# Kernel tuning notes

Measured on AMD Instinct MI355X. Metric: run time of the kernel, lower is better.

## Reference

```python
import jax, jax.numpy as jnp
import numpy as np

HID = 1024
HEADS = 16
HEAD_DIM = HID // HEADS
SCALE = HEAD_DIM ** -0.5


def setup_inputs() -> dict:
    key = jax.random.key(0)
    ks = jax.random.split(key, 11)
    B, S = 4, 2048
    std = HID ** -0.5
    inp = {
        'q': jax.random.normal(ks[0], (B, S, HID), jnp.float32),
        'k': jax.random.normal(ks[1], (B, S, HID), jnp.float32),
        'v': jax.random.normal(ks[2], (B, S, HID), jnp.float32),
        'Wq': jax.random.normal(ks[3], (HID, HID), jnp.float32) * std,
        'bq': jnp.zeros((HID,), jnp.float32),
        'Wk': jax.random.normal(ks[4], (HID, HID), jnp.float32) * std,
        'bk': jnp.zeros((HID,), jnp.float32),
        'Wv': jax.random.normal(ks[5], (HID, HID), jnp.float32) * std,
        'bv': jnp.zeros((HID,), jnp.float32),
        'Wo': jax.random.normal(ks[6], (HID, HID), jnp.float32) * std,
        'bo': jnp.zeros((HID,), jnp.float32),
    }
    return inp


def _split_heads(x, B):
    # [B, S, HID] -> [B, H, S, Dh]
    return x.reshape(B, -1, HEADS, HEAD_DIM).transpose(0, 2, 1, 3)


def reference(q, k, v, Wq, bq, Wk, bk, Wv, bv, Wo, bo):
    B = q.shape[0]
    Q = _split_heads(jnp.dot(q, Wq.T) + bq, B)
    K = _split_heads(jnp.dot(k, Wk.T) + bk, B)
    V = _split_heads(jnp.dot(v, Wv.T) + bv, B)
    # [B, H, Sq, Sk]
    energy = jnp.einsum('bhqd,bhkd->bhqk', Q, K) * SCALE
    attention = jax.nn.softmax(energy, axis=-1)
    x = jnp.einsum('bhqk,bhkd->bhqd', attention, V)  # dropout = identity (eval)
    x = x.transpose(0, 2, 1, 3).reshape(B, -1, HID)
    x = jnp.dot(x, Wo.T) + bo
    return (x, attention)
```

## Files before the change

kernel.cpp:

```cpp
#include <hip/hip_runtime.h>
#include <stdint.h>

#define HID 1024
#define HEADS 16
#define HDIM 64
#define SEQ 2048
#define BATCH 4
#define SCALE 0.125f
#define EXPC 0.18033688011112042f

typedef __bf16 bf16x8 __attribute__((ext_vector_type(8)));
typedef float f32x4 __attribute__((ext_vector_type(4)));
typedef unsigned short ushortx8 __attribute__((ext_vector_type(8)));
typedef unsigned short ushortx4 __attribute__((ext_vector_type(4)));

__device__ __forceinline__ unsigned short f2bf(float f) {
  uint32_t u = __builtin_bit_cast(uint32_t, f);
  u = (u + 0x7fffu + ((u >> 16) & 1u)) >> 16;
  return (unsigned short)u;
}
__device__ __forceinline__ float bf2f(unsigned short u) {
  uint32_t x = ((uint32_t)u) << 16;
  return __builtin_bit_cast(float, x);
}
__device__ __forceinline__ void gl16(const void* g, void* l) {
  __builtin_amdgcn_global_load_lds(
      (const __attribute__((address_space(1))) unsigned int*)g,
      (__attribute__((address_space(3))) unsigned int*)l, 16, 0, 0);
}

struct ConvArgs {
  const float* s[6];
  unsigned short* d[6];
  int n[6];
};
__global__ __launch_bounds__(256) void convk(ConvArgs a) {
  const int ten = blockIdx.y;
  const float* s = a.s[ten];
  unsigned short* d = a.d[ten];
  const int n = a.n[ten];
  const int stride = gridDim.x * blockDim.x * 8;
  for (int i = (blockIdx.x * blockDim.x + threadIdx.x) * 8; i < n; i += stride) {
    float4 v0 = *(const float4*)(s + i);
    float4 v1 = *(const float4*)(s + i + 4);
    ushortx8 o = {f2bf(v0.x), f2bf(v0.y), f2bf(v0.z), f2bf(v0.w),
                  f2bf(v1.x), f2bf(v1.y), f2bf(v1.z), f2bf(v1.w)};
    *(ushortx8*)(d + i) = o;
  }
}

template <int W_F32, int OUT_MODE>
__global__ __launch_bounds__(256) void gemm_bf(
    const unsigned short* __restrict__ A, const void* __restrict__ Wp,
    const float* __restrict__ bias, void* __restrict__ Out) {
  __shared__ unsigned short Als[128 * 64];
  __shared__ unsigned short Bls[128 * 64];
  const int t = threadIdx.x;
  const int bn = blockIdx.x, bm = blockIdx.y;
  const int w = t >> 6, lane = t & 63;
  const int wm = w >> 1, wn = w & 1;
  const int lr = lane & 15, lk = lane >> 4;
  const int row0 = bm * 128, col0 = bn * 128;

  const unsigned short* Abase =
      A + (size_t)(row0 + w * 32 + (lane >> 3)) * HID + (lane & 7) * 8;
  const unsigned short* Wb16 =
      (const unsigned short*)Wp + (size_t)(col0 + w * 32 + (lane >> 3)) * HID +
      (lane & 7) * 8;

  f32x4 acc[4][4] = {};

  for (int ks = 0; ks < 16; ++ks) {
    __syncthreads();
#pragma unroll
    for (int i = 0; i < 4; ++i)
      gl16(Abase + (size_t)i * 8 * HID + ks * 64, &Als[(w * 32 + i * 8) * 64]);
    if (!W_F32) {
#pragma unroll
      for (int i = 0; i < 4; ++i)
        gl16(Wb16 + (size_t)i * 8 * HID + ks * 64, &Bls[(w * 32 + i * 8) * 64]);
    } else {
      const float* Wf = (const float*)Wp;
#pragma unroll
      for (int i = 0; i < 8; ++i) {
        int chunk = t + i * 256;
        int r = chunk >> 4, c4 = (chunk & 15) * 4;
        float4 v4 = *(const float4*)(Wf + (size_t)(col0 + r) * HID + ks * 64 + c4);
        ushortx4 o = {f2bf(v4.x), f2bf(v4.y), f2bf(v4.z), f2bf(v4.w)};
        *(ushortx4*)&Bls[r * 64 + c4] = o;
      }
    }
    __syncthreads();
#pragma unroll
    for (int kk = 0; kk < 2; ++kk) {
      bf16x8 a[4], bb[4];
#pragma unroll
      for (int f = 0; f < 4; ++f) {
        a[f] = *(const bf16x8*)&Als[(wm * 64 + f * 16 + lr) * 64 + kk * 32 + lk * 8];
        bb[f] = *(const bf16x8*)&Bls[(wn * 64 + f * 16 + lr) * 64 + kk * 32 + lk * 8];
      }
#pragma unroll
      for (int fm = 0; fm < 4; ++fm)
#pragma unroll
        for (int fn = 0; fn < 4; ++fn)
          acc[fm][fn] = __builtin_amdgcn_mfma_f32_16x16x32_bf16(
              a[fm], bb[fn], acc[fm][fn], 0, 0, 0);
    }
  }

#pragma unroll
  for (int fn = 0; fn < 4; ++fn) {
    int col = col0 + wn * 64 + fn * 16 + lr;
    float bv = bias[col];
#pragma unroll
    for (int fm = 0; fm < 4; ++fm) {
      int row = row0 + wm * 64 + fm * 16 + lk * 4;
      if (OUT_MODE == 1) {
        int b_ = row >> 11, s = row & 2047;
        int hh = col >> 6, d = col & 63;
        ushortx4 o4 = {f2bf(acc[fm][fn][0] + bv), f2bf(acc[fm][fn][1] + bv),
                       f2bf(acc[fm][fn][2] + bv), f2bf(acc[fm][fn][3] + bv)};
        *(ushortx4*)((unsigned short*)Out +
                     ((size_t)(b_ * HEADS + hh) * HDIM + d) * SEQ + s) = o4;
      } else {
#pragma unroll
        for (int r = 0; r < 4; ++r) {
          float v = acc[fm][fn][r] + bv;
          if (OUT_MODE == 0)
            ((unsigned short*)Out)[(size_t)(row + r) * HID + col] = f2bf(v);
          else
            ((float*)Out)[(size_t)(row + r) * HID + col] = v;
        }
      }
    }
  }
}

__global__ __launch_bounds__(512) void attn_kern(
    const unsigned short* __restrict__ Qb, const unsigned short* __restrict__ Kb,
    const unsigned short* __restrict__ Vt, float* __restrict__ attn_out,
    unsigned short* __restrict__ Xc) {
  __shared__ unsigned short Qls[128][72];
  __shared__ unsigned short Kls[2][64 * 64];
  __shared__ unsigned short Vls[2][64 * 64];

  const int t = threadIdx.x;
  const int qb = blockIdx.x, h = blockIdx.y, b = blockIdx.z;
  const int w = t >> 6, lane = t & 63;
  const int lr = lane & 15, lk = lane >> 4;
  const size_t qrow0 = (size_t)b * SEQ + (size_t)qb * 128;

  const int srow = lane >> 3;
  const int scol = (lane & 7) ^ srow;
  const unsigned short* gK =
      Kb + ((size_t)b * SEQ + w * 8 + srow) * HID + h * HDIM + scol * 8;
  const unsigned short* gV =
      Vt + ((size_t)(b * HEADS + h) * HDIM + w * 8 + srow) * SEQ + scol * 8;
  unsigned short* lK = &Kls[0][w * 8 * 64];
  unsigned short* lV = &Vls[0][w * 8 * 64];

  gl16(gK, lK);

#pragma unroll
  for (int i = 0; i < 2; ++i) {
    int chunk = t + i * 512;
    int r = chunk >> 3, c8 = (chunk & 7) * 8;
    *(ushortx8*)&Qls[r][c8] =
        *(const ushortx8*)(Qb + (qrow0 + r) * HID + h * HDIM + c8);
  }
  __syncthreads();

  bf16x8 qf[2];
#pragma unroll
  for (int kk = 0; kk < 2; ++kk)
    qf[kk] = *(const bf16x8*)&Qls[w * 16 + lr][kk * 32 + lk * 8];
  auto& Pls = Qls;

  float lsum[4] = {0.f, 0.f, 0.f, 0.f};
  int buf = 0;

  for (int kt = 0; kt < 32; ++kt) {
    if (kt < 31) gl16(gK + (size_t)(kt + 1) * 64 * HID, lK + (buf ^ 1) * 4096);
    f32x4 acc[4] = {};
    __builtin_amdgcn_s_setprio(1);
#pragma unroll
    for (int kk = 0; kk < 2; ++kk)
#pragma unroll
      for (int kf = 0; kf < 4; ++kf) {
        bf16x8 bb = *(const bf16x8*)&Kls[buf][(kf * 16 + lr) * 64 +
                                             (((kk * 4 + lk) ^ (lr & 7)) << 3)];
        acc[kf] = __builtin_amdgcn_mfma_f32_16x16x32_bf16(qf[kk], bb, acc[kf], 0, 0, 0);
      }
    __builtin_amdgcn_s_setprio(0);
#pragma unroll
    for (int kf = 0; kf < 4; ++kf)
#pragma unroll
      for (int r = 0; r < 4; ++r) lsum[r] += exp2f(acc[kf][r] * EXPC);
    __syncthreads();
    buf ^= 1;
  }

  float invl[4];
#pragma unroll
  for (int r = 0; r < 4; ++r) {
#pragma unroll
    for (int off = 1; off < 16; off <<= 1) lsum[r] += __shfl_xor(lsum[r], off, 64);
    invl[r] = 1.0f / lsum[r];
  }

  f32x4 oacc[4] = {};
  float* attn_base =
      attn_out + ((size_t)(b * HEADS + h) * SEQ + (size_t)qb * 128) * SEQ;

  gl16(gK, lK);
  gl16(gV, lV);
  __syncthreads();
  for (int kt = 0; kt < 32; ++kt) {
    if (kt < 31) {
      gl16(gK + (size_t)(kt + 1) * 64 * HID, lK + (buf ^ 1) * 4096);
      gl16(gV + (size_t)(kt + 1) * 64, lV + (buf ^ 1) * 4096);
    }
    f32x4 acc[4] = {};
    __builtin_amdgcn_s_setprio(1);
#pragma unroll
    for (int kk = 0; kk < 2; ++kk)
#pragma unroll
      for (int kf = 0; kf < 4; ++kf) {
        bf16x8 bb = *(const bf16x8*)&Kls[buf][(kf * 16 + lr) * 64 +
                                             (((kk * 4 + lk) ^ (lr & 7)) << 3)];
        acc[kf] = __builtin_amdgcn_mfma_f32_16x16x32_bf16(qf[kk], bb, acc[kf], 0, 0, 0);
      }
    __builtin_amdgcn_s_setprio(0);
#pragma unroll
    for (int kf = 0; kf < 4; ++kf)
#pragma unroll
      for (int r = 0; r < 4; ++r) {
        float p = exp2f(acc[kf][r] * EXPC) * invl[r];
        Pls[w * 16 + lk * 4 + r][kf * 16 + lr] = f2bf(p);
      }
#pragma unroll
    for (int it = 0; it < 4; ++it) {
      int rl = it * 4 + lk;
      ushortx4 p4 = *(const ushortx4*)&Pls[w * 16 + rl][lr * 4];
      f32x4 o = {bf2f(p4[0]), bf2f(p4[1]), bf2f(p4[2]), bf2f(p4[3])};
      __builtin_nontemporal_store(
          o, (f32x4*)(attn_base + (size_t)(w * 16 + rl) * SEQ + kt * 64 + lr * 4));
    }
    __builtin_amdgcn_s_setprio(1);
#pragma unroll
    for (int kk = 0; kk < 2; ++kk) {
      bf16x8 ap = *(const bf16x8*)&Pls[w * 16 + lr][kk * 32 + lk * 8];
#pragma unroll
      for (int df = 0; df < 4; ++df) {
        bf16x8 bv = *(const bf16x8*)&Vls[buf][(df * 16 + lr) * 64 +
                                             (((kk * 4 + lk) ^ (lr & 7)) << 3)];
        oacc[df] = __builtin_amdgcn_mfma_f32_16x16x32_bf16(ap, bv, oacc[df], 0, 0, 0);
      }
    }
    __builtin_amdgcn_s_setprio(0);
    __syncthreads();
    buf ^= 1;
  }

#pragma unroll
  for (int df = 0; df < 4; ++df)
#pragma unroll
    for (int r = 0; r < 4; ++r) {
      int row = w * 16 + lk * 4 + r;
      int col = h * HDIM + df * 16 + lr;
      Xc[(qrow0 + row) * HID + col] = f2bf(oacc[df][r]);
    }
}

extern "C" void kernel_launch(void* const* d_in, const int* in_sizes, int n_in,
                              void* d_out, int out_size, void* d_ws, size_t ws_size,
                              hipStream_t stream) {
  const float* q = (const float*)d_in[0];
  const float* k = (const float*)d_in[1];
  const float* v = (const float*)d_in[2];
  const float* Wq = (const float*)d_in[3];
  const float* bq = (const float*)d_in[4];
  const float* Wk = (const float*)d_in[5];
  const float* bk = (const float*)d_in[6];
  const float* Wv = (const float*)d_in[7];
  const float* bv = (const float*)d_in[8];
  const float* Wo = (const float*)d_in[9];
  const float* bo = (const float*)d_in[10];

  char* ws = (char*)d_ws;
  const size_t MAT = (size_t)8192 * 1024 * sizeof(unsigned short);
  unsigned short* Qbuf = (unsigned short*)(ws);
  unsigned short* Kbuf = (unsigned short*)(ws + MAT);
  unsigned short* Vtb = (unsigned short*)(ws + 2 * MAT);
  unsigned short* Xc = (unsigned short*)(ws + 3 * MAT);

  float* xout = (float*)d_out;
  float* attn_out = xout + (size_t)BATCH * SEQ * HID;

  unsigned short* scr = (unsigned short*)attn_out;
  const int NQ = 8192 * 1024, NW = 1024 * 1024;
  unsigned short* qb16 = scr;
  unsigned short* kb16 = scr + (size_t)NQ;
  unsigned short* vb16 = scr + (size_t)2 * NQ;
  unsigned short* wq16 = scr + (size_t)3 * NQ;
  unsigned short* wk16 = wq16 + NW;
  unsigned short* wv16 = wk16 + NW;

  ConvArgs ca;
  ca.s[0] = q; ca.s[1] = k; ca.s[2] = v; ca.s[3] = Wq; ca.s[4] = Wk; ca.s[5] = Wv;
  ca.d[0] = qb16; ca.d[1] = kb16; ca.d[2] = vb16;
  ca.d[3] = wq16; ca.d[4] = wk16; ca.d[5] = wv16;
  ca.n[0] = NQ; ca.n[1] = NQ; ca.n[2] = NQ;
  ca.n[3] = NW; ca.n[4] = NW; ca.n[5] = NW;

  dim3 blk(256);
  hipLaunchKernelGGL(convk, dim3(512, 6), blk, 0, stream, ca);
  dim3 gp(8, 64);
  hipLaunchKernelGGL((gemm_bf<0, 0>), gp, blk, 0, stream, qb16, wq16, bq, Qbuf);
  hipLaunchKernelGGL((gemm_bf<0, 0>), gp, blk, 0, stream, kb16, wk16, bk, Kbuf);
  hipLaunchKernelGGL((gemm_bf<0, 1>), gp, blk, 0, stream, vb16, wv16, bv, Vtb);
  hipLaunchKernelGGL((attn_kern), dim3(16, 16, 4), dim3(512), 0, stream, Qbuf, Kbuf,
                     Vtb, attn_out, Xc);
  hipLaunchKernelGGL((gemm_bf<1, 2>), gp, blk, 0, stream, Xc, Wo, bo, xout);
}
```

Measured before the change: 460.4 us.

## Merge QKV GEMMs, remap attention blocks per XCD, pre-convert Wo to bf16

```diff
diff --git a/kernel.cpp b/kernel.cpp
--- a/kernel.cpp
+++ b/kernel.cpp
@@ -30,9 +30,9 @@
 }
 
 struct ConvArgs {
-  const float* s[6];
-  unsigned short* d[6];
-  int n[6];
+  const float* s[7];
+  unsigned short* d[7];
+  int n[7];
 };
 __global__ __launch_bounds__(256) void convk(ConvArgs a) {
   const int ten = blockIdx.y;
@@ -49,10 +49,87 @@
   }
 }
 
-template <int W_F32, int OUT_MODE>
-__global__ __launch_bounds__(256) void gemm_bf(
+struct QkvArgs {
+  const unsigned short* A[3];
+  const unsigned short* W[3];
+  const float* bias[3];
+  unsigned short* out[3];
+};
+__global__ __launch_bounds__(256) void gemm_qkv(QkvArgs ar) {
+  __shared__ unsigned short Als[128 * 64];
+  __shared__ unsigned short Bls[128 * 64];
+  const int z = blockIdx.z;
+  const unsigned short* A = ar.A[z];
+  const unsigned short* Wb = ar.W[z];
+  const float* bias = ar.bias[z];
+  unsigned short* Out = ar.out[z];
+
+  const int t = threadIdx.x;
+  const int bn = blockIdx.x, bm = blockIdx.y;
+  const int w = t >> 6, lane = t & 63;
+  const int wm = w >> 1, wn = w & 1;
+  const int lr = lane & 15, lk = lane >> 4;
+  const int row0 = bm * 128, col0 = bn * 128;
+
+  const unsigned short* Abase =
+      A + (size_t)(row0 + w * 32 + (lane >> 3)) * HID + (lane & 7) * 8;
+  const unsigned short* Wbase =
+      Wb + (size_t)(col0 + w * 32 + (lane >> 3)) * HID + (lane & 7) * 8;
+
+  f32x4 acc[4][4] = {};
+
+  for (int ks = 0; ks < 16; ++ks) {
+    __syncthreads();
+#pragma unroll
+    for (int i = 0; i < 4; ++i)
+      gl16(Abase + (size_t)i * 8 * HID + ks * 64, &Als[(w * 32 + i * 8) * 64]);
+#pragma unroll
+    for (int i = 0; i < 4; ++i)
+      gl16(Wbase + (size_t)i * 8 * HID + ks * 64, &Bls[(w * 32 + i * 8) * 64]);
+    __syncthreads();
+#pragma unroll
+    for (int kk = 0; kk < 2; ++kk) {
+      bf16x8 a[4], bb[4];
+#pragma unroll
+      for (int f = 0; f < 4; ++f) {
+        a[f] = *(const bf16x8*)&Als[(wm * 64 + f * 16 + lr) * 64 + kk * 32 + lk * 8];
+        bb[f] = *(const bf16x8*)&Bls[(wn * 64 + f * 16 + lr) * 64 + kk * 32 + lk * 8];
+      }
+#pragma unroll
+      for (int fm = 0; fm < 4; ++fm)
+#pragma unroll
+        for (int fn = 0; fn < 4; ++fn)
+          acc[fm][fn] = __builtin_amdgcn_mfma_f32_16x16x32_bf16(
+              a[fm], bb[fn], acc[fm][fn], 0, 0, 0);
+    }
+  }
+
+#pragma unroll
+  for (int fn = 0; fn < 4; ++fn) {
+    int col = col0 + wn * 64 + fn * 16 + lr;
+    float bv = bias[col];
+#pragma unroll
+    for (int fm = 0; fm < 4; ++fm) {
+      int row = row0 + wm * 64 + fm * 16 + lk * 4;
+      if (z == 2) {
+        int b_ = row >> 11, s = row & 2047;
+        int hh = col >> 6, d = col & 63;
+        ushortx4 o4 = {f2bf(acc[fm][fn][0] + bv), f2bf(acc[fm][fn][1] + bv),
+                       f2bf(acc[fm][fn][2] + bv), f2bf(acc[fm][fn][3] + bv)};
+        *(ushortx4*)(Out + ((size_t)(b_ * HEADS + hh) * HDIM + d) * SEQ + s) = o4;
+      } else {
+#pragma unroll
+        for (int r = 0; r < 4; ++r)
+          Out[(size_t)(row + r) * HID + col] = f2bf(acc[fm][fn][r] + bv);
+      }
+    }
+  }
+}
+
+template <int W_F32>
+__global__ __launch_bounds__(256) void gemm_wo(
     const unsigned short* __restrict__ A, const void* __restrict__ Wp,
-    const float* __restrict__ bias, void* __restrict__ Out) {
+    const float* __restrict__ bias, float* __restrict__ Out) {
   __shared__ unsigned short Als[128 * 64];
   __shared__ unsigned short Bls[128 * 64];
   const int t = threadIdx.x;
@@ -115,23 +192,9 @@
 #pragma unroll
     for (int fm = 0; fm < 4; ++fm) {
       int row = row0 + wm * 64 + fm * 16 + lk * 4;
-      if (OUT_MODE == 1) {
-        int b_ = row >> 11, s = row & 2047;
-        int hh = col >> 6, d = col & 63;
-        ushortx4 o4 = {f2bf(acc[fm][fn][0] + bv), f2bf(acc[fm][fn][1] + bv),
-                       f2bf(acc[fm][fn][2] + bv), f2bf(acc[fm][fn][3] + bv)};
-        *(ushortx4*)((unsigned short*)Out +
-                     ((size_t)(b_ * HEADS + hh) * HDIM + d) * SEQ + s) = o4;
-      } else {
-#pragma unroll
-        for (int r = 0; r < 4; ++r) {
-          float v = acc[fm][fn][r] + bv;
-          if (OUT_MODE == 0)
-            ((unsigned short*)Out)[(size_t)(row + r) * HID + col] = f2bf(v);
-          else
-            ((float*)Out)[(size_t)(row + r) * HID + col] = v;
-        }
-      }
+#pragma unroll
+      for (int r = 0; r < 4; ++r)
+        Out[(size_t)(row + r) * HID + col] = acc[fm][fn][r] + bv;
     }
   }
 }
@@ -145,10 +208,14 @@
   __shared__ unsigned short Vls[2][64 * 64];
 
   const int t = threadIdx.x;
-  const int qb = blockIdx.x, h = blockIdx.y, b = blockIdx.z;
+  const int bid = blockIdx.x;
+  const int wgid = (bid & 7) * 64 + (bid >> 3);
+  const int qbp = wgid & 7;
+  const int h = (wgid >> 3) & 15;
+  const int b = wgid >> 7;
+
   const int w = t >> 6, lane = t & 63;
   const int lr = lane & 15, lk = lane >> 4;
-  const size_t qrow0 = (size_t)b * SEQ + (size_t)qb * 128;
 
   const int srow = lane >> 3;
   const int scol = (lane & 7) ^ srow;
@@ -159,117 +226,123 @@
   unsigned short* lK = &Kls[0][w * 8 * 64];
   unsigned short* lV = &Vls[0][w * 8 * 64];
 
-  gl16(gK, lK);
-
-#pragma unroll
-  for (int i = 0; i < 2; ++i) {
-    int chunk = t + i * 512;
-    int r = chunk >> 3, c8 = (chunk & 7) * 8;
-    *(ushortx8*)&Qls[r][c8] =
-        *(const ushortx8*)(Qb + (qrow0 + r) * HID + h * HDIM + c8);
-  }
-  __syncthreads();
-
-  bf16x8 qf[2];
-#pragma unroll
-  for (int kk = 0; kk < 2; ++kk)
-    qf[kk] = *(const bf16x8*)&Qls[w * 16 + lr][kk * 32 + lk * 8];
-  auto& Pls = Qls;
-
-  float lsum[4] = {0.f, 0.f, 0.f, 0.f};
-  int buf = 0;
-
-  for (int kt = 0; kt < 32; ++kt) {
-    if (kt < 31) gl16(gK + (size_t)(kt + 1) * 64 * HID, lK + (buf ^ 1) * 4096);
-    f32x4 acc[4] = {};
-    __builtin_amdgcn_s_setprio(1);
+  for (int qbi = 0; qbi < 2; ++qbi) {
+    const int qb = qbp * 2 + qbi;
+    const size_t qrow0 = (size_t)b * SEQ + (size_t)qb * 128;
+
+    gl16(gK, lK);
+#pragma unroll
+    for (int i = 0; i < 2; ++i) {
+      int chunk = t + i * 512;
+      int r = chunk >> 3, c8 = (chunk & 7) * 8;
+      *(ushortx8*)&Qls[r][c8] =
+          *(const ushortx8*)(Qb + (qrow0 + r) * HID + h * HDIM + c8);
+    }
+    __syncthreads();
+
+    bf16x8 qf[2];
 #pragma unroll
     for (int kk = 0; kk < 2; ++kk)
-#pragma unroll
-      for (int kf = 0; kf < 4; ++kf) {
-        bf16x8 bb = *(const bf16x8*)&Kls[buf][(kf * 16 + lr) * 64 +
-                                             (((kk * 4 + lk) ^ (lr & 7)) << 3)];
-        acc[kf] = __builtin_amdgcn_mfma_f32_16x16x32_bf16(qf[kk], bb, acc[kf], 0, 0, 0);
-      }
-    __builtin_amdgcn_s_setprio(0);
-#pragma unroll
-    for (int kf = 0; kf < 4; ++kf)
-#pragma unroll
-      for (int r = 0; r < 4; ++r) lsum[r] += exp2f(acc[kf][r] * EXPC);
-    __syncthreads();
-    buf ^= 1;
-  }
-
-  float invl[4];
-#pragma unroll
-  for (int r = 0; r < 4; ++r) {
-#pragma unroll
-    for (int off = 1; off < 16; off <<= 1) lsum[r] += __shfl_xor(lsum[r], off, 64);
-    invl[r] = 1.0f / lsum[r];
-  }
-
-  f32x4 oacc[4] = {};
-  float* attn_base =
-      attn_out + ((size_t)(b * HEADS + h) * SEQ + (size_t)qb * 128) * SEQ;
-
-  gl16(gK, lK);
-  gl16(gV, lV);
-  __syncthreads();
-  for (int kt = 0; kt < 32; ++kt) {
-    if (kt < 31) {
-      gl16(gK + (size_t)(kt + 1) * 64 * HID, lK + (buf ^ 1) * 4096);
-      gl16(gV + (size_t)(kt + 1) * 64, lV + (buf ^ 1) * 4096);
-    }
-    f32x4 acc[4] = {};
-    __builtin_amdgcn_s_setprio(1);
-#pragma unroll
-    for (int kk = 0; kk < 2; ++kk)
-#pragma unroll
-      for (int kf = 0; kf < 4; ++kf) {
-        bf16x8 bb = *(const bf16x8*)&Kls[buf][(kf * 16 + lr) * 64 +
-                                             (((kk * 4 + lk) ^ (lr & 7)) << 3)];
-        acc[kf] = __builtin_amdgcn_mfma_f32_16x16x32_bf16(qf[kk], bb, acc[kf], 0, 0, 0);
-      }
-    __builtin_amdgcn_s_setprio(0);
-#pragma unroll
-    for (int kf = 0; kf < 4; ++kf)
+      qf[kk] = *(const bf16x8*)&Qls[w * 16 + lr][kk * 32 + lk * 8];
+    auto& Pls = Qls;
+
+    float lsum[4] = {0.f, 0.f, 0.f, 0.f};
+    int buf = 0;
+
+    for (int kt = 0; kt < 32; ++kt) {
+      if (kt < 31) gl16(gK + (size_t)(kt + 1) * 64 * HID, lK + (buf ^ 1) * 4096);
+      f32x4 acc[4] = {};
+      __builtin_amdgcn_s_setprio(1);
+#pragma unroll
+      for (int kk = 0; kk < 2; ++kk)
+#pragma unroll
+        for (int kf = 0; kf < 4; ++kf) {
+          bf16x8 bb = *(const bf16x8*)&Kls[buf][(kf * 16 + lr) * 64 +
+                                               (((kk * 4 + lk) ^ (lr & 7)) << 3)];
+          acc[kf] =
+              __builtin_amdgcn_mfma_f32_16x16x32_bf16(qf[kk], bb, acc[kf], 0, 0, 0);
+        }
+      __builtin_amdgcn_s_setprio(0);
+#pragma unroll
+      for (int kf = 0; kf < 4; ++kf)
+#pragma unroll
+        for (int r = 0; r < 4; ++r) lsum[r] += exp2f(acc[kf][r] * EXPC);
+      __syncthreads();
+      buf ^= 1;
+    }
+
+    float invl[4];
+#pragma unroll
+    for (int r = 0; r < 4; ++r) {
+#pragma unroll
+      for (int off = 1; off < 16; off <<= 1) lsum[r] += __shfl_xor(lsum[r], off, 64);
+      invl[r] = 1.0f / lsum[r];
+    }
+
+    f32x4 oacc[4] = {};
+    float* attn_base =
+        attn_out + ((size_t)(b * HEADS + h) * SEQ + (size_t)qb * 128) * SEQ;
+
+    gl16(gK, lK);
+    gl16(gV, lV);
+    __syncthreads();
+    for (int kt = 0; kt < 32; ++kt) {
+      if (kt < 31) {
+        gl16(gK + (size_t)(kt + 1) * 64 * HID, lK + (buf ^ 1) * 4096);
+        gl16(gV + (size_t)(kt + 1) * 64, lV + (buf ^ 1) * 4096);
+      }
+      f32x4 acc[4] = {};
+      __builtin_amdgcn_s_setprio(1);
+#pragma unroll
+      for (int kk = 0; kk < 2; ++kk)
+#pragma unroll
+        for (int kf = 0; kf < 4; ++kf) {
+          bf16x8 bb = *(const bf16x8*)&Kls[buf][(kf * 16 + lr) * 64 +
+                                               (((kk * 4 + lk) ^ (lr & 7)) << 3)];
+          acc[kf] =
+              __builtin_amdgcn_mfma_f32_16x16x32_bf16(qf[kk], bb, acc[kf], 0, 0, 0);
+        }
+      __builtin_amdgcn_s_setprio(0);
+#pragma unroll
+      for (int kf = 0; kf < 4; ++kf)
+#pragma unroll
+        for (int r = 0; r < 4; ++r) {
+          float p = exp2f(acc[kf][r] * EXPC) * invl[r];
+          Pls[w * 16 + lk * 4 + r][kf * 16 + lr] = f2bf(p);
+        }
+#pragma unroll
+      for (int it = 0; it < 4; ++it) {
+        int rl = it * 4 + lk;
+        ushortx4 p4 = *(const ushortx4*)&Pls[w * 16 + rl][lr * 4];
+        f32x4 o = {bf2f(p4[0]), bf2f(p4[1]), bf2f(p4[2]), bf2f(p4[3])};
+        __builtin_nontemporal_store(
+            o, (f32x4*)(attn_base + (size_t)(w * 16 + rl) * SEQ + kt * 64 + lr * 4));
+      }
+      __builtin_amdgcn_s_setprio(1);
+#pragma unroll
+      for (int kk = 0; kk < 2; ++kk) {
+        bf16x8 ap = *(const bf16x8*)&Pls[w * 16 + lr][kk * 32 + lk * 8];
+#pragma unroll
+        for (int df = 0; df < 4; ++df) {
+          bf16x8 bv = *(const bf16x8*)&Vls[buf][(df * 16 + lr) * 64 +
+                                               (((kk * 4 + lk) ^ (lr & 7)) << 3)];
+          oacc[df] = __builtin_amdgcn_mfma_f32_16x16x32_bf16(ap, bv, oacc[df], 0, 0, 0);
+        }
+      }
+      __builtin_amdgcn_s_setprio(0);
+      __syncthreads();
+      buf ^= 1;
+    }
+
+#pragma unroll
+    for (int df = 0; df < 4; ++df)
 #pragma unroll
       for (int r = 0; r < 4; ++r) {
-        float p = exp2f(acc[kf][r] * EXPC) * invl[r];
-        Pls[w * 16 + lk * 4 + r][kf * 16 + lr] = f2bf(p);
-      }
-#pragma unroll
-    for (int it = 0; it < 4; ++it) {
-      int rl = it * 4 + lk;
-      ushortx4 p4 = *(const ushortx4*)&Pls[w * 16 + rl][lr * 4];
-      f32x4 o = {bf2f(p4[0]), bf2f(p4[1]), bf2f(p4[2]), bf2f(p4[3])};
-      __builtin_nontemporal_store(
-          o, (f32x4*)(attn_base + (size_t)(w * 16 + rl) * SEQ + kt * 64 + lr * 4));
-    }
-    __builtin_amdgcn_s_setprio(1);
-#pragma unroll
-    for (int kk = 0; kk < 2; ++kk) {
-      bf16x8 ap = *(const bf16x8*)&Pls[w * 16 + lr][kk * 32 + lk * 8];
-#pragma unroll
-      for (int df = 0; df < 4; ++df) {
-        bf16x8 bv = *(const bf16x8*)&Vls[buf][(df * 16 + lr) * 64 +
-                                             (((kk * 4 + lk) ^ (lr & 7)) << 3)];
-        oacc[df] = __builtin_amdgcn_mfma_f32_16x16x32_bf16(ap, bv, oacc[df], 0, 0, 0);
-      }
-    }
-    __builtin_amdgcn_s_setprio(0);
-    __syncthreads();
-    buf ^= 1;
-  }
-
-#pragma unroll
-  for (int df = 0; df < 4; ++df)
-#pragma unroll
-    for (int r = 0; r < 4; ++r) {
-      int row = w * 16 + lk * 4 + r;
-      int col = h * HDIM + df * 16 + lr;
-      Xc[(qrow0 + row) * HID + col] = f2bf(oacc[df][r]);
-    }
+        int row = w * 16 + lk * 4 + r;
+        int col = h * HDIM + df * 16 + lr;
+        Xc[(qrow0 + row) * HID + col] = f2bf(oacc[df][r]);
+      }
+  }
 }
 
 extern "C" void kernel_launch(void* const* d_in, const int* in_sizes, int n_in,
@@ -305,21 +378,33 @@
   unsigned short* wq16 = scr + (size_t)3 * NQ;
   unsigned short* wk16 = wq16 + NW;
   unsigned short* wv16 = wk16 + NW;
+  unsigned short* wo16 = (unsigned short*)(ws + 4 * MAT);
+  const bool wo_bf = ws_size >= 4 * MAT + (size_t)NW * sizeof(unsigned short);
 
   ConvArgs ca;
-  ca.s[0] = q; ca.s[1] = k; ca.s[2] = v; ca.s[3] = Wq; ca.s[4] = Wk; ca.s[5] = Wv;
+  ca.s[0] = q;  ca.s[1] = k;  ca.s[2] = v;
+  ca.s[3] = Wq; ca.s[4] = Wk; ca.s[5] = Wv; ca.s[6] = Wo;
   ca.d[0] = qb16; ca.d[1] = kb16; ca.d[2] = vb16;
-  ca.d[3] = wq16; ca.d[4] = wk16; ca.d[5] = wv16;
+  ca.d[3] = wq16; ca.d[4] = wk16; ca.d[5] = wv16; ca.d[6] = wo16;
   ca.n[0] = NQ; ca.n[1] = NQ; ca.n[2] = NQ;
-  ca.n[3] = NW; ca.n[4] = NW; ca.n[5] = NW;
+  ca.n[3] = NW; ca.n[4] = NW; ca.n[5] = NW; ca.n[6] = NW;
 
   dim3 blk(256);
-  hipLaunchKernelGGL(convk, dim3(512, 6), blk, 0, stream, ca);
+  hipLaunchKernelGGL(convk, dim3(512, wo_bf ? 7 : 6), blk, 0, stream, ca);
+
+  QkvArgs qa;
+  qa.A[0] = qb16; qa.A[1] = kb16; qa.A[2] = vb16;
+  qa.W[0] = wq16; qa.W[1] = wk16; qa.W[2] = wv16;
+  qa.bias[0] = bq; qa.bias[1] = bk; qa.bias[2] = bv;
+  qa.out[0] = Qbuf; qa.out[1] = Kbuf; qa.out[2] = Vtb;
+  hipLaunchKernelGGL(gemm_qkv, dim3(8, 64, 3), blk, 0, stream, qa);
+
+  hipLaunchKernelGGL(attn_kern, dim3(512), dim3(512), 0, stream, Qbuf, Kbuf, Vtb,
+                     attn_out, Xc);
+
   dim3 gp(8, 64);
-  hipLaunchKernelGGL((gemm_bf<0, 0>), gp, blk, 0, stream, qb16, wq16, bq, Qbuf);
-  hipLaunchKernelGGL((gemm_bf<0, 0>), gp, blk, 0, stream, kb16, wk16, bk, Kbuf);
-  hipLaunchKernelGGL((gemm_bf<0, 1>), gp, blk, 0, stream, vb16, wv16, bv, Vtb);
-  hipLaunchKernelGGL((attn_kern), dim3(16, 16, 4), dim3(512), 0, stream, Qbuf, Kbuf,
-                     Vtb, attn_out, Xc);
-  hipLaunchKernelGGL((gemm_bf<1, 2>), gp, blk, 0, stream, Xc, Wo, bo, xout);
-}
+  if (wo_bf)
+    hipLaunchKernelGGL((gemm_wo<0>), gp, blk, 0, stream, Xc, wo16, bo, xout);
+  else
+    hipLaunchKernelGGL((gemm_wo<1>), gp, blk, 0, stream, Xc, Wo, bo, xout);
+}
```

After: 417.7 us. 1.1x faster.
